# Optimization experiments

Measured on AMD Instinct MI355X. Metric: run time of the kernel, lower is better.

The kernel has to match this reference:

```python
import jax, jax.numpy as jnp
import numpy as np


def setup_inputs() -> dict:
    key = jax.random.key(0)
    k1, k2 = jax.random.split(key)
    imgs = jax.random.normal(k1, (8, 32, 256, 256), dtype=jnp.float32)
    kernel = jax.random.normal(k2, (32, 1, 5, 5), dtype=jnp.float32)
    return {
        "imgs": imgs,
        "kernel": kernel,
        "stride": 1,
        "padding": 2,
        "dilation": 1,
        "groups": 32,
    }


def reference(imgs, kernel, stride, padding, dilation, groups):
    """Tropical (max-plus) select-semifield convolution (correlation layout).

    out[b, oc, oy, ox] = max over (g, ky, kx) of
        imgs[b, ic, oy*stride - pad + ky*dil, ox*stride - pad + kx*dil]
        + kernel[oc_in_group, g, ky, kx]
    with ic = (oc // per_group_out) * krn_cs + g. Out-of-bounds taps are
    skipped (neutral element -inf), matching the CUDA kernel's bounds check.
    """
    B, C, H, W = imgs.shape
    OC, KC, KY, KX = kernel.shape  # KC = krn_cs = C // groups
    per_group_out = OC // groups
    out_h = (H + 2 * padding - dilation * (KY - 1) - 1) // stride + 1
    out_w = (W + 2 * padding - dilation * (KX - 1) - 1) // stride + 1

    neutral = -jnp.inf  # semifield neutral for max-plus
    padded = jnp.pad(
        imgs,
        ((0, 0), (0, 0), (padding, padding), (padding, padding)),
        constant_values=neutral,
    )

    oc = jnp.arange(OC)
    acc = jnp.full((B, OC, out_h, out_w), neutral, dtype=imgs.dtype)
    for g in range(KC):  # fixed small loop over kernel taps (krn_cs * KY * KX)
        ic = (oc // per_group_out) * KC + g
        img_g = padded[:, ic]  # [B, OC, H+2p, W+2p] aligned to output channels
        for ky in range(KY):
            ys = slice(ky * dilation, ky * dilation + stride * (out_h - 1) + 1, stride)
            for kx in range(KX):
                xs = slice(kx * dilation, kx * dilation + stride * (out_w - 1) + 1, stride)
                k = kernel[:, g, ky, kx][None, :, None, None]  # [1, OC, 1, 1]
                acc = jnp.maximum(acc, img_g[:, :, ys, xs] + k)
    return acc
```

## Files before the change

### kernel.cpp

```cpp
#include <hip/hip_runtime.h>
#include <math.h>

#define BB 8
#define CC 32
#define HH 256
#define WW 256
#define PAD 2

__global__ __launch_bounds__(256) void selconv_kernel(
    const float* __restrict__ imgs,
    const float* __restrict__ kern,
    float* __restrict__ out)
{
    const int t   = threadIdx.x;
    const int gid = blockIdx.x * 256 + t;
    const int xq  = gid & 63;
    const int rt  = (gid >> 6) & 31;
    const int p   = gid >> 11;
    const int c   = p & (CC - 1);
    const int x   = xq * 4;
    const int y0  = rt * 8;

    float w[25];
    const float* kw = kern + c * 25;
#pragma unroll
    for (int i = 0; i < 25; ++i) w[i] = kw[i];

    const float NEG = -INFINITY;
    const float* plane = imgs + (size_t)p * (HH * WW);

    float acc[8][4];
#pragma unroll
    for (int r = 0; r < 8; ++r)
#pragma unroll
        for (int j = 0; j < 4; ++j) acc[r][j] = NEG;

#pragma unroll
    for (int iyo = -2; iyo < 10; ++iyo) {
        const int iy = y0 + iyo;
        if (iy < 0 || iy >= HH) continue;
        const float* rp = plane + iy * WW;

        float4 va = (x - 4 >= 0) ? *reinterpret_cast<const float4*>(rp + x - 4)
                                 : make_float4(NEG, NEG, NEG, NEG);
        float4 vb = *reinterpret_cast<const float4*>(rp + x);
        float4 vc = (x + 4 < WW) ? *reinterpret_cast<const float4*>(rp + x + 4)
                                 : make_float4(NEG, NEG, NEG, NEG);
        const float v[12] = {va.x, va.y, va.z, va.w,
                             vb.x, vb.y, vb.z, vb.w,
                             vc.x, vc.y, vc.z, vc.w};

#pragma unroll
        for (int r = 0; r < 8; ++r) {
            const int ky = iyo - r + 2;
            if (ky < 0 || ky > 4) continue;
#pragma unroll
            for (int j = 0; j < 4; ++j) {
                const float m0 = v[2 + j] + w[ky * 5 + 0];
                const float m1 = v[3 + j] + w[ky * 5 + 1];
                const float m2 = v[4 + j] + w[ky * 5 + 2];
                const float m3 = v[5 + j] + w[ky * 5 + 3];
                const float m4 = v[6 + j] + w[ky * 5 + 4];
                acc[r][j] = fmaxf(acc[r][j],
                                  fmaxf(fmaxf(fmaxf(m0, m1), m2), fmaxf(m3, m4)));
            }
        }
    }

    float* op = out + (size_t)p * (HH * WW) + y0 * WW + x;
#pragma unroll
    for (int r = 0; r < 8; ++r) {
        *reinterpret_cast<float4*>(op + r * WW) =
            make_float4(acc[r][0], acc[r][1], acc[r][2], acc[r][3]);
    }
}

extern "C" void kernel_launch(void* const* d_in, const int* in_sizes, int n_in,
                              void* d_out, int out_size, void* d_ws, size_t ws_size,
                              hipStream_t stream)
{
    const float* imgs = (const float*)d_in[0];
    const float* kern = (const float*)d_in[1];
    float* out = (float*)d_out;

    const int blocks = (BB * CC * (HH / 8) * (WW / 4)) / 256;
    selconv_kernel<<<blocks, 256, 0, stream>>>(imgs, kern, out);
}
```

Before: 31.54 us.

## Widen per-thread tile to 8x8 and pair kernel rows with packed f32x2 adds

Each thread now computes an 8x8 output tile instead of 8x4, so block count drops fourfold and each loaded input row feeds more outputs with less halo overhead. Kernel rows are paired into two-wide vectors so one packed add serves two output rows, aiming at v_pk_add_f32 on CDNA. The cost is more registers per thread (64 accumulators plus 16 inputs), which may lower occupancy, and fewer total threads, leaving less parallelism to hide latency.

```diff
diff --git a/kernel.cpp b/kernel.cpp
--- a/kernel.cpp
+++ b/kernel.cpp
@@ -5,64 +5,109 @@
 #define CC 32
 #define HH 256
 #define WW 256
-#define PAD 2
+
+typedef float f32x2 __attribute__((ext_vector_type(2)));
 
 __global__ __launch_bounds__(256) void selconv_kernel(
     const float* __restrict__ imgs,
     const float* __restrict__ kern,
     float* __restrict__ out)
 {
-    const int t   = threadIdx.x;
-    const int gid = blockIdx.x * 256 + t;
-    const int xq  = gid & 63;
-    const int rt  = (gid >> 6) & 31;
-    const int p   = gid >> 11;
-    const int c   = p & (CC - 1);
-    const int x   = xq * 4;
-    const int y0  = rt * 8;
+    const int t    = threadIdx.x;
+    const int p    = blockIdx.x >> 2;
+    const int blky = blockIdx.x & 3;
+    const int c    = p & (CC - 1);
+    const int x    = (t & 31) * 8;
+    const int y0   = blky * 64 + (t >> 5) * 8;
 
     float w[25];
     const float* kw = kern + c * 25;
 #pragma unroll
     for (int i = 0; i < 25; ++i) w[i] = kw[i];
 
+    f32x2 wp[2][5];
+#pragma unroll
+    for (int k = 0; k < 5; ++k) {
+        wp[0][k] = f32x2{w[20 + k], w[15 + k]};
+        wp[1][k] = f32x2{w[10 + k], w[5 + k]};
+    }
+
     const float NEG = -INFINITY;
     const float* plane = imgs + (size_t)p * (HH * WW);
 
-    float acc[8][4];
+    float acc[8][8];
 #pragma unroll
     for (int r = 0; r < 8; ++r)
 #pragma unroll
-        for (int j = 0; j < 4; ++j) acc[r][j] = NEG;
+        for (int j = 0; j < 8; ++j) acc[r][j] = NEG;
 
 #pragma unroll
-    for (int iyo = -2; iyo < 10; ++iyo) {
+    for (int iyo = -2; iyo <= 9; ++iyo) {
         const int iy = y0 + iyo;
         if (iy < 0 || iy >= HH) continue;
         const float* rp = plane + iy * WW;
 
-        float4 va = (x - 4 >= 0) ? *reinterpret_cast<const float4*>(rp + x - 4)
+        float V[16];
+        {
+            float4 q0 = (x >= 4) ? *reinterpret_cast<const float4*>(rp + x - 4)
                                  : make_float4(NEG, NEG, NEG, NEG);
-        float4 vb = *reinterpret_cast<const float4*>(rp + x);
-        float4 vc = (x + 4 < WW) ? *reinterpret_cast<const float4*>(rp + x + 4)
-                                 : make_float4(NEG, NEG, NEG, NEG);
-        const float v[12] = {va.x, va.y, va.z, va.w,
-                             vb.x, vb.y, vb.z, vb.w,
-                             vc.x, vc.y, vc.z, vc.w};
+            float4 q1 = *reinterpret_cast<const float4*>(rp + x);
+            float4 q2 = *reinterpret_cast<const float4*>(rp + x + 4);
+            float4 q3 = (x + 8 < WW) ? *reinterpret_cast<const float4*>(rp + x + 8)
+                                     : make_float4(NEG, NEG, NEG, NEG);
+            V[0]=q0.x; V[1]=q0.y; V[2]=q0.z; V[3]=q0.w;
+            V[4]=q1.x; V[5]=q1.y; V[6]=q1.z; V[7]=q1.w;
+            V[8]=q2.x; V[9]=q2.y; V[10]=q2.z; V[11]=q2.w;
+            V[12]=q3.x; V[13]=q3.y; V[14]=q3.z; V[15]=q3.w;
+        }
 
 #pragma unroll
-        for (int r = 0; r < 8; ++r) {
-            const int ky = iyo - r + 2;
-            if (ky < 0 || ky > 4) continue;
+        for (int kp = 0; kp < 2; ++kp) {
+            const int kyA = 4 - kp * 2;
+            const int kyB = kyA - 1;
+            const int rA  = iyo - kyA + 2;
+            const int rB  = iyo - kyB + 2;
+            const bool vA = (rA >= 0) && (rA <= 7);
+            const bool vB = (rB >= 0) && (rB <= 7);
+            if (vA && vB) {
 #pragma unroll
-            for (int j = 0; j < 4; ++j) {
-                const float m0 = v[2 + j] + w[ky * 5 + 0];
-                const float m1 = v[3 + j] + w[ky * 5 + 1];
-                const float m2 = v[4 + j] + w[ky * 5 + 2];
-                const float m3 = v[5 + j] + w[ky * 5 + 3];
-                const float m4 = v[6 + j] + w[ky * 5 + 4];
-                acc[r][j] = fmaxf(acc[r][j],
-                                  fmaxf(fmaxf(fmaxf(m0, m1), m2), fmaxf(m3, m4)));
+                for (int j = 0; j < 8; ++j) {
+                    f32x2 m0 = f32x2{V[2+j], V[2+j]} + wp[kp][0];
+                    f32x2 m1 = f32x2{V[3+j], V[3+j]} + wp[kp][1];
+                    f32x2 m2 = f32x2{V[4+j], V[4+j]} + wp[kp][2];
+                    f32x2 m3 = f32x2{V[5+j], V[5+j]} + wp[kp][3];
+                    f32x2 m4 = f32x2{V[6+j], V[6+j]} + wp[kp][4];
+                    float ax = acc[rA][j];
+                    ax = fmaxf(fmaxf(ax, m0.x), m1.x);
+                    ax = fmaxf(fmaxf(ax, m2.x), m3.x);
+                    acc[rA][j] = fmaxf(ax, m4.x);
+                    float ay = acc[rB][j];
+                    ay = fmaxf(fmaxf(ay, m0.y), m1.y);
+                    ay = fmaxf(fmaxf(ay, m2.y), m3.y);
+                    acc[rB][j] = fmaxf(ay, m4.y);
+                }
+            } else if (vA || vB) {
+                const int ky = vA ? kyA : kyB;
+                const int r  = vA ? rA : rB;
+#pragma unroll
+                for (int j = 0; j < 8; ++j) {
+                    float a = acc[r][j];
+                    a = fmaxf(fmaxf(a, V[2+j] + w[ky*5+0]), V[3+j] + w[ky*5+1]);
+                    a = fmaxf(fmaxf(a, V[4+j] + w[ky*5+2]), V[5+j] + w[ky*5+3]);
+                    acc[r][j] = fmaxf(a, V[6+j] + w[ky*5+4]);
+                }
+            }
+        }
+        {
+            const int r = iyo + 2;
+            if (r >= 0 && r <= 7) {
+#pragma unroll
+                for (int j = 0; j < 8; ++j) {
+                    float a = acc[r][j];
+                    a = fmaxf(fmaxf(a, V[2+j] + w[0]), V[3+j] + w[1]);
+                    a = fmaxf(fmaxf(a, V[4+j] + w[2]), V[5+j] + w[3]);
+                    acc[r][j] = fmaxf(a, V[6+j] + w[4]);
+                }
             }
         }
     }
@@ -72,6 +117,8 @@
     for (int r = 0; r < 8; ++r) {
         *reinterpret_cast<float4*>(op + r * WW) =
             make_float4(acc[r][0], acc[r][1], acc[r][2], acc[r][3]);
+        *reinterpret_cast<float4*>(op + r * WW + 4) =
+            make_float4(acc[r][4], acc[r][5], acc[r][6], acc[r][7]);
     }
 }
 
@@ -83,6 +130,6 @@
     const float* kern = (const float*)d_in[1];
     float* out = (float*)d_out;
 
-    const int blocks = (BB * CC * (HH / 8) * (WW / 4)) / 256;
+    const int blocks = BB * CC * 4;
     selconv_kernel<<<blocks, 256, 0, stream>>>(imgs, kern, out);
 }
```

New measurement: 36.40 us. +15.4%, slower.

## Double-buffer row loads, make wave indices uniform, and clamp edge loads

Applied to the files above, without the earlier changes.

Adds software double-buffering, so the next input row's loads are issued before the current row's max-plus work. Remaps the thread index so each wave's plane and row-tile are wave-uniform via readfirstlane, which makes the kernel weights scalar loads. Replaces the conditional edge loads with clamped unconditional loads plus selects, and adds a launch-bounds occupancy hint of 6. The extra buffers raise register pressure and may cut occupancy, which could offset the overlap gain.

```diff
diff --git a/kernel.cpp b/kernel.cpp
--- a/kernel.cpp
+++ b/kernel.cpp
@@ -5,21 +5,20 @@
 #define CC 32
 #define HH 256
 #define WW 256
-#define PAD 2
 
-__global__ __launch_bounds__(256) void selconv_kernel(
+__global__ __launch_bounds__(256, 6) void selconv_kernel(
     const float* __restrict__ imgs,
     const float* __restrict__ kern,
     float* __restrict__ out)
 {
-    const int t   = threadIdx.x;
-    const int gid = blockIdx.x * 256 + t;
-    const int xq  = gid & 63;
-    const int rt  = (gid >> 6) & 31;
-    const int p   = gid >> 11;
-    const int c   = p & (CC - 1);
-    const int x   = xq * 4;
-    const int y0  = rt * 8;
+    const int t    = threadIdx.x;
+    const int lane = t & 63;
+    const int wave = __builtin_amdgcn_readfirstlane(blockIdx.x * 4 + (t >> 6));
+    const int p    = wave >> 5;
+    const int rt   = wave & 31;
+    const int c    = p & (CC - 1);
+    const int y0   = rt * 8;
+    const int x    = lane * 4;
 
     float w[25];
     const float* kw = kern + c * 25;
@@ -29,42 +28,60 @@
     const float NEG = -INFINITY;
     const float* plane = imgs + (size_t)p * (HH * WW);
 
+    const bool okL = (x >= 4);
+    const bool okR = (x + 4 < WW);
+    const int  xm4 = okL ? x - 4 : 0;
+    const int  xp4 = okR ? x + 4 : x;
+
     float acc[8][4];
 #pragma unroll
     for (int r = 0; r < 8; ++r)
 #pragma unroll
         for (int j = 0; j < 4; ++j) acc[r][j] = NEG;
 
+    float bufA[12], bufB[12];
+
+    auto loadrow = [&](float* buf, int iyo) {
+        const int iy = y0 + iyo;
+        if (iy < 0 || iy >= HH) return;
+        const float* rp = plane + iy * WW;
+        float4 qa = *reinterpret_cast<const float4*>(rp + xm4);
+        float4 qb = *reinterpret_cast<const float4*>(rp + x);
+        float4 qc = *reinterpret_cast<const float4*>(rp + xp4);
+        buf[0] = okL ? qa.x : NEG;  buf[1] = okL ? qa.y : NEG;
+        buf[2] = okL ? qa.z : NEG;  buf[3] = okL ? qa.w : NEG;
+        buf[4] = qb.x;  buf[5] = qb.y;  buf[6] = qb.z;  buf[7] = qb.w;
+        buf[8]  = okR ? qc.x : NEG; buf[9]  = okR ? qc.y : NEG;
+        buf[10] = okR ? qc.z : NEG; buf[11] = okR ? qc.w : NEG;
+    };
+
+    auto computerow = [&](const float* buf, int iyo) {
+        const int iy = y0 + iyo;
+        if (iy < 0 || iy >= HH) return;
 #pragma unroll
-    for (int iyo = -2; iyo < 10; ++iyo) {
-        const int iy = y0 + iyo;
-        if (iy < 0 || iy >= HH) continue;
-        const float* rp = plane + iy * WW;
-
-        float4 va = (x - 4 >= 0) ? *reinterpret_cast<const float4*>(rp + x - 4)
-                                 : make_float4(NEG, NEG, NEG, NEG);
-        float4 vb = *reinterpret_cast<const float4*>(rp + x);
-        float4 vc = (x + 4 < WW) ? *reinterpret_cast<const float4*>(rp + x + 4)
-                                 : make_float4(NEG, NEG, NEG, NEG);
-        const float v[12] = {va.x, va.y, va.z, va.w,
-                             vb.x, vb.y, vb.z, vb.w,
-                             vc.x, vc.y, vc.z, vc.w};
-
-#pragma unroll
-        for (int r = 0; r < 8; ++r) {
-            const int ky = iyo - r + 2;
-            if (ky < 0 || ky > 4) continue;
+        for (int ky = 0; ky < 5; ++ky) {
+            const int r = iyo + 2 - ky;
+            if (r < 0 || r > 7) continue;
 #pragma unroll
             for (int j = 0; j < 4; ++j) {
-                const float m0 = v[2 + j] + w[ky * 5 + 0];
-                const float m1 = v[3 + j] + w[ky * 5 + 1];
-                const float m2 = v[4 + j] + w[ky * 5 + 2];
-                const float m3 = v[5 + j] + w[ky * 5 + 3];
-                const float m4 = v[6 + j] + w[ky * 5 + 4];
-                acc[r][j] = fmaxf(acc[r][j],
-                                  fmaxf(fmaxf(fmaxf(m0, m1), m2), fmaxf(m3, m4)));
+                const float s0 = buf[2 + j] + w[ky * 5 + 0];
+                const float s1 = buf[3 + j] + w[ky * 5 + 1];
+                const float s2 = buf[4 + j] + w[ky * 5 + 2];
+                const float s3 = buf[5 + j] + w[ky * 5 + 3];
+                const float s4 = buf[6 + j] + w[ky * 5 + 4];
+                acc[r][j] = fmaxf(fmaxf(fmaxf(s0, s1), s2),
+                                  fmaxf(fmaxf(s3, s4), acc[r][j]));
             }
         }
+    };
+
+    loadrow(bufA, -2);
+#pragma unroll
+    for (int s = -2; s <= 9; ++s) {
+        float* cur = ((s + 2) & 1) ? bufB : bufA;
+        float* nxt = ((s + 3) & 1) ? bufB : bufA;
+        if (s < 9) loadrow(nxt, s + 1);
+        computerow(cur, s);
     }
 
     float* op = out + (size_t)p * (HH * WW) + y0 * WW + x;
```

Measured after the change: 40.08 us. 1.27x slower.
